# Optimization experiments

Measured on AMD Instinct MI355X. Metric: run time of the kernel, lower is better.

Reference implementation:

```python
import jax, jax.numpy as jnp
import numpy as np

N = 100000   # nodes in batched graph
E = 1600000  # edges (before self-loops)
D = 128      # in_dim == hidden_dim == num_outputs
G = 64       # graphs in the batch


def setup_inputs() -> dict:
    key = jax.random.key(0)
    ks = jax.random.split(key, 8)
    s = 1.0 / np.sqrt(D)
    x = jax.random.normal(ks[0], (N, D), jnp.float32)
    src = jax.random.randint(ks[1], (E,), 0, N, dtype=jnp.int64)
    dst = jax.random.randint(ks[2], (E,), 0, N, dtype=jnp.int64)
    graph_ids = jnp.sort(jax.random.randint(ks[3], (N,), 0, G, dtype=jnp.int64))
    W0 = jax.random.normal(ks[4], (D, D), jnp.float32) * s
    W1 = jax.random.normal(ks[5], (D, D), jnp.float32) * s
    W2 = jax.random.normal(ks[6], (D, D), jnp.float32) * s
    b0 = jnp.zeros((D,), jnp.float32)
    b1 = jnp.zeros((D,), jnp.float32)
    b2 = jnp.zeros((D,), jnp.float32)
    return {"x": x, "W0": W0, "b0": b0, "W1": W1, "b1": b1,
            "W2": W2, "b2": b2, "src": src, "dst": dst, "graph_ids": graph_ids}


def reference(x, W0, b0, W1, b1, W2, b2, src, dst, graph_ids):
    n = x.shape[0]
    loops = jnp.arange(n, dtype=src.dtype)
    src_f = jnp.concatenate([src, loops])  # add self-loops once (dgl.add_self_loop)
    dst_f = jnp.concatenate([dst, loops])
    ones_e = jnp.ones(src_f.shape, x.dtype)
    deg_out = jax.ops.segment_sum(ones_e, src_f, num_segments=n)  # >=1 (self-loop)
    deg_in = jax.ops.segment_sum(ones_e, dst_f, num_segments=n)
    cs = jax.lax.rsqrt(deg_out)[:, None]  # source norm (GraphConv norm='both')
    cd = jax.lax.rsqrt(deg_in)[:, None]   # destination norm

    def gcn_layer(h, W, b):
        m = (h * cs)[src_f]                                   # [E+N, D] gather
        agg = jax.ops.segment_sum(m, dst_f, num_segments=n)   # scatter-add SpMM
        return jax.nn.relu((agg * cd) @ W + b)                # F.relu(conv(g, h))

    h = gcn_layer(x, W0, b0)
    h = gcn_layer(h, W1, b1)
    h = gcn_layer(h, W2, b2)

    # dgl.mean_nodes: per-graph mean over nodes
    sums = jax.ops.segment_sum(h, graph_ids, num_segments=G)
    cnt = jax.ops.segment_sum(jnp.ones((n, 1), h.dtype), graph_ids, num_segments=G)
    return sums / jnp.maximum(cnt, 1.0)  # [G, D] logits
```

## Files before the change

### kernel.cpp

```cpp
#include <hip/hip_runtime.h>
#include <stdint.h>

#define D 128
#define CAP 64
#define HB 128
#define CH 25000

typedef __attribute__((ext_vector_type(8))) short bf16x8;
typedef __attribute__((ext_vector_type(4))) float f32x4;

__device__ inline unsigned short f2bf(float x) {
  union { float f; uint32_t u; } v; v.f = x;
  uint32_t u = v.u;
  u += 0x7fffu + ((u >> 16) & 1u);
  return (unsigned short)(u >> 16);
}
__device__ inline float bflo(uint32_t u) {
  union { uint32_t u; float f; } v; v.u = u << 16; return v.f;
}
__device__ inline float bfhi(uint32_t u) {
  union { uint32_t u; float f; } v; v.u = u & 0xffff0000u; return v.f;
}
__device__ inline uint32_t packbf(float lo, float hi) {
  return (uint32_t)f2bf(lo) | ((uint32_t)f2bf(hi) << 16);
}

__global__ __launch_bounds__(256) void hist_kernel(
    const int* __restrict__ src, const int* __restrict__ dst,
    unsigned int* __restrict__ parts_s, unsigned int* __restrict__ parts_d,
    int E, int N,
    const float* __restrict__ W0, const float* __restrict__ W1,
    const float* __restrict__ W2, unsigned short* __restrict__ Wt,
    int* __restrict__ cnt, int G, float* __restrict__ outz, int out_total) {
  __shared__ unsigned int lbs[CH / 8];
  __shared__ unsigned int lbd[CH / 8];
  int b = blockIdx.x & (HB - 1);
  int lo = (blockIdx.x >> 7) * CH;
  for (int i = threadIdx.x; i < CH / 8; i += 256) { lbs[i] = 0; lbd[i] = 0; }
  __syncthreads();
  int per = (E + HB - 1) / HB;
  int e0 = b * per;
  int e1 = min(e0 + per, E);
  for (int e = e0 + threadIdx.x; e < e1; e += 256) {
    int rs = src[e] - lo;
    if ((unsigned)rs < CH) atomicAdd(&lbs[rs >> 3], 1u << ((rs & 7) * 4));
    int rd = dst[e] - lo;
    if ((unsigned)rd < CH) atomicAdd(&lbd[rd >> 3], 1u << ((rd & 7) * 4));
  }
  __syncthreads();
  int nu = (N + 7) / 8;
  int base = lo >> 3;
  int cu = min(CH / 8, nu - base);
  unsigned int* ps = parts_s + (size_t)b * nu + base;
  unsigned int* pd = parts_d + (size_t)b * nu + base;
  for (int i = threadIdx.x; i < cu; i += 256) { ps[i] = lbs[i]; pd[i] = lbd[i]; }

  int gs = gridDim.x * 256;
  for (int i = blockIdx.x * 256 + threadIdx.x; i < 3 * 16384; i += gs) {
    int l = i >> 14, r = i & 16383;
    int n = r >> 7, k = r & 127;
    const float* W = (l == 0) ? W0 : (l == 1) ? W1 : W2;
    Wt[i] = f2bf(W[k * 128 + n]);
  }
  for (int i = blockIdx.x * 256 + threadIdx.x; i < G; i += gs) cnt[i] = 0;
  for (int i = blockIdx.x * 256 + threadIdx.x; i < out_total; i += gs) outz[i] = 0.f;
}

__global__ __launch_bounds__(256) void scan_norm_kernel(
    const unsigned char* __restrict__ parts_s,
    const unsigned char* __restrict__ parts_d,
    unsigned char* __restrict__ offs_d,
    int* __restrict__ degd,
    float* __restrict__ cs, float* __restrict__ cd,
    const int* __restrict__ gid, int* __restrict__ cnt,
    int N, int G) {
  __shared__ int lcnt[256];
  for (int i = threadIdx.x; i < G; i += 256) lcnt[i] = 0;
  __syncthreads();

  int t = blockIdx.x * blockDim.x + threadIdx.x;
  int i0 = t * 2;
  if (i0 < N) {
    int nb = N / 2;
    int ds0 = 0, ds1 = 0, dd0 = 0, dd1 = 0;
    for (int b = 0; b < HB; b++) {
      unsigned char sv = parts_s[(size_t)b * nb + t];
      ds0 += sv & 15; ds1 += sv >> 4;
      unsigned char dv = parts_d[(size_t)b * nb + t];
      offs_d[(size_t)b * N + i0]     = (unsigned char)min(dd0, 255);
      offs_d[(size_t)b * N + i0 + 1] = (unsigned char)min(dd1, 255);
      dd0 += dv & 15; dd1 += dv >> 4;
    }
    degd[i0] = dd0;     degd[i0 + 1] = dd1;
    cs[i0] = rsqrtf((float)ds0 + 1.0f);
    cs[i0 + 1] = rsqrtf((float)ds1 + 1.0f);
    cd[i0] = rsqrtf((float)dd0 + 1.0f);
    cd[i0 + 1] = rsqrtf((float)dd1 + 1.0f);
    atomicAdd(&lcnt[gid[i0]], 1);
    if (i0 + 1 < N) atomicAdd(&lcnt[gid[i0 + 1]], 1);
  }
  __syncthreads();
  for (int i = threadIdx.x; i < G; i += 256) {
    int c = lcnt[i];
    if (c) atomicAdd(&cnt[i], c);
  }
}

__global__ __launch_bounds__(256) void fill_kernel(
    const int* __restrict__ src, const int* __restrict__ dst,
    const unsigned char* __restrict__ offs_d, int* __restrict__ col, int E, int N,
    const float* __restrict__ x, const float* __restrict__ cs,
    uint32_t* __restrict__ xs) {
  __shared__ unsigned int lcur[CH / 8];
  int b = blockIdx.x & (HB - 1);
  int lo = (blockIdx.x >> 7) * CH;
  for (int i = threadIdx.x; i < CH / 8; i += 256) lcur[i] = 0;
  __syncthreads();
  int per = (E + HB - 1) / HB;
  int e0 = b * per;
  int e1 = min(e0 + per, E);
  const unsigned char* offb = offs_d + (size_t)b * N;
  for (int e = e0 + threadIdx.x; e < e1; e += 256) {
    int d = dst[e];
    int rd = d - lo;
    if ((unsigned)rd < CH) {
      unsigned old = atomicAdd(&lcur[rd >> 3], 1u << ((rd & 7) * 4));
      int local = (old >> ((rd & 7) * 4)) & 0xF;
      int pos = (int)offb[d] + local;
      if (pos < CAP) col[(size_t)d * CAP + pos] = src[e];
    }
  }
  int total2 = N * 64;
  int gs = gridDim.x * 256;
  for (int i = blockIdx.x * 256 + threadIdx.x; i < total2; i += gs) {
    float2 v = ((const float2*)x)[i];
    float c = cs[i >> 6];
    xs[i] = packbf(v.x * c, v.y * c);
  }
}

__global__ __launch_bounds__(512) void fused_layer_kernel(
    const uint32_t* __restrict__ hin, const unsigned short* __restrict__ Wt,
    const float* __restrict__ bias, const float* __restrict__ cd,
    const float* __restrict__ rowscale, const int* __restrict__ degd,
    const int* __restrict__ col, unsigned short* __restrict__ hout, int N) {
  __shared__ __align__(16) uint32_t At[16 * 68];

  int wv = threadIdx.x >> 6;
  int lane = threadIdx.x & 63;
  int m = lane & 15;
  int quad = lane >> 4;

  bf16x8 bfr[4];
#pragma unroll
  for (int c = 0; c < 4; c++)
    bfr[c] = *(const bf16x8*)(Wt + (size_t)(16 * wv + m) * 128 + c * 32 + quad * 8);

#pragma unroll
  for (int j = 0; j < 2; j++) {
    int w = __builtin_amdgcn_readfirstlane(blockIdx.x * 16 + wv * 2 + j);
    float accx = 0.f, accy = 0.f;
    if (w < N) {
      int n = min(degd[w], CAP);
      const int* cw = col + (size_t)w * CAP;
      const uint32_t* hl = hin + lane;
      uint32_t selfv = hl[(size_t)w * 64];
      accx = bflo(selfv); accy = bfhi(selfv);
      int i = 0;
      for (; i + 7 < n; i += 8) {
        int s0 = cw[i],     s1 = cw[i + 1], s2 = cw[i + 2], s3 = cw[i + 3];
        int s4 = cw[i + 4], s5 = cw[i + 5], s6 = cw[i + 6], s7 = cw[i + 7];
        uint32_t v0 = hl[(size_t)s0 * 64];
        uint32_t v1 = hl[(size_t)s1 * 64];
        uint32_t v2 = hl[(size_t)s2 * 64];
        uint32_t v3 = hl[(size_t)s3 * 64];
        uint32_t v4 = hl[(size_t)s4 * 64];
        uint32_t v5 = hl[(size_t)s5 * 64];
        uint32_t v6 = hl[(size_t)s6 * 64];
        uint32_t v7 = hl[(size_t)s7 * 64];
        accx += bflo(v0); accy += bfhi(v0);
        accx += bflo(v1); accy += bfhi(v1);
        accx += bflo(v2); accy += bfhi(v2);
        accx += bflo(v3); accy += bfhi(v3);
        accx += bflo(v4); accy += bfhi(v4);
        accx += bflo(v5); accy += bfhi(v5);
        accx += bflo(v6); accy += bfhi(v6);
        accx += bflo(v7); accy += bfhi(v7);
      }
      for (; i + 3 < n; i += 4) {
        int s0 = cw[i], s1 = cw[i + 1], s2 = cw[i + 2], s3 = cw[i + 3];
        uint32_t v0 = hl[(size_t)s0 * 64];
        uint32_t v1 = hl[(size_t)s1 * 64];
        uint32_t v2 = hl[(size_t)s2 * 64];
        uint32_t v3 = hl[(size_t)s3 * 64];
        accx += bflo(v0); accy += bfhi(v0);
        accx += bflo(v1); accy += bfhi(v1);
        accx += bflo(v2); accy += bfhi(v2);
        accx += bflo(v3); accy += bfhi(v3);
      }
      for (; i < n; i++) {
        uint32_t v = hl[(size_t)cw[i] * 64];
        accx += bflo(v); accy += bfhi(v);
      }
      float cdv = cd[w];
      accx *= cdv; accy *= cdv;
    }
    At[(wv * 2 + j) * 68 + lane] = packbf(accx, accy);
  }
  __syncthreads();

  const unsigned short* arow = (const unsigned short*)At + m * 136;
  f32x4 acc = f32x4{0.f, 0.f, 0.f, 0.f};
#pragma unroll
  for (int c = 0; c < 4; c++) {
    bf16x8 a = *(const bf16x8*)(arow + c * 32 + quad * 8);
    acc = __builtin_amdgcn_mfma_f32_16x16x32_bf16(a, bfr[c], acc, 0, 0, 0);
  }
  int colb = 16 * wv + m;
  float bv = bias[colb];
#pragma unroll
  for (int i = 0; i < 4; i++) {
    int r = blockIdx.x * 16 + quad * 4 + i;
    if (r < N) {
      float v = acc[i] + bv;
      v = v > 0.f ? v : 0.f;
      if (rowscale) v *= rowscale[r];
      hout[(size_t)r * D + colb] = f2bf(v);
    }
  }
}

__global__ void pool_kernel(const unsigned short* __restrict__ h, const int* __restrict__ gid,
                            float* __restrict__ outsum, const int* __restrict__ cnt, int N) {
  int v0 = blockIdx.x * 64;
  if (v0 >= N) return;
  int d = threadIdx.x;
  int vend = min(v0 + 64, N);
  int cur = gid[v0];
  float acc = 0.f;
  for (int v = v0; v < vend; v++) {
    int g = gid[v];
    if (g != cur) {
      float inv = 1.0f / fmaxf((float)cnt[cur], 1.0f);
      atomicAdd(&outsum[cur * D + d], acc * inv);
      acc = 0.f; cur = g;
    }
    unsigned short hv = __builtin_nontemporal_load(&h[(size_t)v * D + d]);
    union { uint32_t u; float f; } cv; cv.u = (uint32_t)hv << 16;
    acc += cv.f;
  }
  float inv = 1.0f / fmaxf((float)cnt[cur], 1.0f);
  atomicAdd(&outsum[cur * D + d], acc * inv);
}

extern "C" void kernel_launch(void* const* d_in, const int* in_sizes, int n_in,
                              void* d_out, int out_size, void* d_ws, size_t ws_size,
                              hipStream_t stream) {
  const float* x  = (const float*)d_in[0];
  const float* W0 = (const float*)d_in[1];
  const float* b0 = (const float*)d_in[2];
  const float* W1 = (const float*)d_in[3];
  const float* b1 = (const float*)d_in[4];
  const float* W2 = (const float*)d_in[5];
  const float* b2 = (const float*)d_in[6];
  const int* src  = (const int*)d_in[7];
  const int* dst  = (const int*)d_in[8];
  const int* gid  = (const int*)d_in[9];

  const int N = in_sizes[0] / D;
  const int E = in_sizes[7];
  const int G = out_size / D;
  const int nu = (N + 7) / 8;

  uint32_t* hsA = (uint32_t*)d_ws;
  uint32_t* hsB = hsA + (size_t)N * 64;
  int* col      = (int*)(hsB + (size_t)N * 64);
  int* degd     = col + (size_t)N * CAP;
  float* csb    = (float*)(degd + N);
  float* cdb    = csb + N;
  int* cnt      = (int*)(cdb + N);
  unsigned short* Wt = (unsigned short*)(cnt + G);
  unsigned int* parts_s = (unsigned int*)(Wt + 3 * 16384);
  unsigned int* parts_d = parts_s + (size_t)HB * nu;
  unsigned char* offs_d = (unsigned char*)(parts_d + (size_t)HB * nu);

  const int nch = (N + CH - 1) / CH;
  hist_kernel<<<HB * nch, 256, 0, stream>>>(src, dst, parts_s, parts_d, E, N,
                                            W0, W1, W2, Wt, cnt, G,
                                            (float*)d_out, out_size);
  scan_norm_kernel<<<(N / 2 + 255) / 256, 256, 0, stream>>>(
      (const unsigned char*)parts_s, (const unsigned char*)parts_d, offs_d,
      degd, csb, cdb, gid, cnt, N, G);
  fill_kernel<<<HB * nch, 256, 0, stream>>>(src, dst, offs_d, col, E, N, x, csb, hsA);

  const int ltiles = (N + 15) / 16;

  fused_layer_kernel<<<ltiles, 512, 0, stream>>>(hsA, Wt, b0, cdb, csb, degd, col,
                                                 (unsigned short*)hsB, N);
  fused_layer_kernel<<<ltiles, 512, 0, stream>>>(hsB, Wt + 16384, b1, cdb, csb, degd, col,
                                                 (unsigned short*)hsA, N);
  fused_layer_kernel<<<ltiles, 512, 0, stream>>>(hsA, Wt + 2 * 16384, b2, cdb, nullptr, degd, col,
                                                 (unsigned short*)hsB, N);

  pool_kernel<<<(N + 63) / 64, 128, 0, stream>>>((const unsigned short*)hsB, gid,
                                                 (float*)d_out, cnt, N);
}
```

Measured before the change: 454.1 us.

## Build adjacency with global atomics and broadcast neighbor indices via readlane

Replaces the three-kernel shared-memory histogram, scan and fill pipeline with a single kernel that uses global atomics to count degrees and place source indices into the capped per-destination column lists, plus a fused normalisation, x-scaling and weight-transpose kernel. The layer kernel now loads each node's 64 neighbor indices once per wave and broadcasts them with readlane, interleaving two destination rows to overlap their gathers, and it uses nontemporal stores for outputs. This removes kernel launches and the partition scratch traffic, at the cost of heavy global atomic contention and a nondeterministic neighbor order.

```diff
diff --git a/kernel.cpp b/kernel.cpp
--- a/kernel.cpp
+++ b/kernel.cpp
@@ -3,8 +3,6 @@
 
 #define D 128
 #define CAP 64
-#define HB 128
-#define CH 25000
 
 typedef __attribute__((ext_vector_type(8))) short bf16x8;
 typedef __attribute__((ext_vector_type(4))) float f32x4;
@@ -25,121 +23,71 @@
   return (uint32_t)f2bf(lo) | ((uint32_t)f2bf(hi) << 16);
 }
 
-__global__ __launch_bounds__(256) void hist_kernel(
+__global__ __launch_bounds__(256) void build_kernel(
     const int* __restrict__ src, const int* __restrict__ dst,
-    unsigned int* __restrict__ parts_s, unsigned int* __restrict__ parts_d,
-    int E, int N,
+    int* __restrict__ degs, int* __restrict__ degd, int* __restrict__ col, int E) {
+  int t = blockIdx.x * 256 + threadIdx.x;
+  int gs = gridDim.x * 256;
+  int half = E >> 1;
+  for (int i = t; i < half; i += gs) {
+    int2 s2 = ((const int2*)src)[i];
+    int2 d2 = ((const int2*)dst)[i];
+    atomicAdd(&degs[s2.x], 1);
+    atomicAdd(&degs[s2.y], 1);
+    int p0 = atomicAdd(&degd[d2.x], 1);
+    if (p0 < CAP) col[(size_t)d2.x * CAP + p0] = s2.x;
+    int p1 = atomicAdd(&degd[d2.y], 1);
+    if (p1 < CAP) col[(size_t)d2.y * CAP + p1] = s2.y;
+  }
+  if (t == 0 && (E & 1)) {
+    int e = E - 1;
+    int s = src[e], d = dst[e];
+    atomicAdd(&degs[s], 1);
+    int p = atomicAdd(&degd[d], 1);
+    if (p < CAP) col[(size_t)d * CAP + p] = s;
+  }
+}
+
+__global__ __launch_bounds__(256) void norm_x_kernel(
+    const float* __restrict__ x, const int* __restrict__ degs,
+    const int* __restrict__ degd, float* __restrict__ cs, float* __restrict__ cd,
+    uint2* __restrict__ xs4, const int* __restrict__ gid, int* __restrict__ cnt,
+    int N, int G,
     const float* __restrict__ W0, const float* __restrict__ W1,
-    const float* __restrict__ W2, unsigned short* __restrict__ Wt,
-    int* __restrict__ cnt, int G, float* __restrict__ outz, int out_total) {
-  __shared__ unsigned int lbs[CH / 8];
-  __shared__ unsigned int lbd[CH / 8];
-  int b = blockIdx.x & (HB - 1);
-  int lo = (blockIdx.x >> 7) * CH;
-  for (int i = threadIdx.x; i < CH / 8; i += 256) { lbs[i] = 0; lbd[i] = 0; }
+    const float* __restrict__ W2, unsigned short* __restrict__ Wt) {
+  __shared__ int lcnt[256];
+  int t = blockIdx.x * 256 + threadIdx.x;
+  int gs = gridDim.x * 256;
+  for (int i = threadIdx.x; i < G; i += 256) lcnt[i] = 0;
   __syncthreads();
-  int per = (E + HB - 1) / HB;
-  int e0 = b * per;
-  int e1 = min(e0 + per, E);
-  for (int e = e0 + threadIdx.x; e < e1; e += 256) {
-    int rs = src[e] - lo;
-    if ((unsigned)rs < CH) atomicAdd(&lbs[rs >> 3], 1u << ((rs & 7) * 4));
-    int rd = dst[e] - lo;
-    if ((unsigned)rd < CH) atomicAdd(&lbd[rd >> 3], 1u << ((rd & 7) * 4));
+  for (int i = t; i < N; i += gs) {
+    cs[i] = rsqrtf((float)degs[i] + 1.0f);
+    cd[i] = rsqrtf((float)degd[i] + 1.0f);
+    atomicAdd(&lcnt[gid[i]], 1);
   }
   __syncthreads();
-  int nu = (N + 7) / 8;
-  int base = lo >> 3;
-  int cu = min(CH / 8, nu - base);
-  unsigned int* ps = parts_s + (size_t)b * nu + base;
-  unsigned int* pd = parts_d + (size_t)b * nu + base;
-  for (int i = threadIdx.x; i < cu; i += 256) { ps[i] = lbs[i]; pd[i] = lbd[i]; }
-
-  int gs = gridDim.x * 256;
-  for (int i = blockIdx.x * 256 + threadIdx.x; i < 3 * 16384; i += gs) {
+  for (int i = threadIdx.x; i < G; i += 256) {
+    int c = lcnt[i];
+    if (c) atomicAdd(&cnt[i], c);
+  }
+  int tot = N * 32;
+  for (int i = t; i < tot; i += gs) {
+    float4 v = ((const float4*)x)[i];
+    float c = rsqrtf((float)degs[i >> 5] + 1.0f);
+    uint2 o;
+    o.x = packbf(v.x * c, v.y * c);
+    o.y = packbf(v.z * c, v.w * c);
+    xs4[i] = o;
+  }
+  for (int i = t; i < 3 * 16384; i += gs) {
     int l = i >> 14, r = i & 16383;
     int n = r >> 7, k = r & 127;
     const float* W = (l == 0) ? W0 : (l == 1) ? W1 : W2;
     Wt[i] = f2bf(W[k * 128 + n]);
   }
-  for (int i = blockIdx.x * 256 + threadIdx.x; i < G; i += gs) cnt[i] = 0;
-  for (int i = blockIdx.x * 256 + threadIdx.x; i < out_total; i += gs) outz[i] = 0.f;
-}
-
-__global__ __launch_bounds__(256) void scan_norm_kernel(
-    const unsigned char* __restrict__ parts_s,
-    const unsigned char* __restrict__ parts_d,
-    unsigned char* __restrict__ offs_d,
-    int* __restrict__ degd,
-    float* __restrict__ cs, float* __restrict__ cd,
-    const int* __restrict__ gid, int* __restrict__ cnt,
-    int N, int G) {
-  __shared__ int lcnt[256];
-  for (int i = threadIdx.x; i < G; i += 256) lcnt[i] = 0;
-  __syncthreads();
-
-  int t = blockIdx.x * blockDim.x + threadIdx.x;
-  int i0 = t * 2;
-  if (i0 < N) {
-    int nb = N / 2;
-    int ds0 = 0, ds1 = 0, dd0 = 0, dd1 = 0;
-    for (int b = 0; b < HB; b++) {
-      unsigned char sv = parts_s[(size_t)b * nb + t];
-      ds0 += sv & 15; ds1 += sv >> 4;
-      unsigned char dv = parts_d[(size_t)b * nb + t];
-      offs_d[(size_t)b * N + i0]     = (unsigned char)min(dd0, 255);
-      offs_d[(size_t)b * N + i0 + 1] = (unsigned char)min(dd1, 255);
-      dd0 += dv & 15; dd1 += dv >> 4;
-    }
-    degd[i0] = dd0;     degd[i0 + 1] = dd1;
-    cs[i0] = rsqrtf((float)ds0 + 1.0f);
-    cs[i0 + 1] = rsqrtf((float)ds1 + 1.0f);
-    cd[i0] = rsqrtf((float)dd0 + 1.0f);
-    cd[i0 + 1] = rsqrtf((float)dd1 + 1.0f);
-    atomicAdd(&lcnt[gid[i0]], 1);
-    if (i0 + 1 < N) atomicAdd(&lcnt[gid[i0 + 1]], 1);
-  }
-  __syncthreads();
-  for (int i = threadIdx.x; i < G; i += 256) {
-    int c = lcnt[i];
-    if (c) atomicAdd(&cnt[i], c);
-  }
-}
-
-__global__ __launch_bounds__(256) void fill_kernel(
-    const int* __restrict__ src, const int* __restrict__ dst,
-    const unsigned char* __restrict__ offs_d, int* __restrict__ col, int E, int N,
-    const float* __restrict__ x, const float* __restrict__ cs,
-    uint32_t* __restrict__ xs) {
-  __shared__ unsigned int lcur[CH / 8];
-  int b = blockIdx.x & (HB - 1);
-  int lo = (blockIdx.x >> 7) * CH;
-  for (int i = threadIdx.x; i < CH / 8; i += 256) lcur[i] = 0;
-  __syncthreads();
-  int per = (E + HB - 1) / HB;
-  int e0 = b * per;
-  int e1 = min(e0 + per, E);
-  const unsigned char* offb = offs_d + (size_t)b * N;
-  for (int e = e0 + threadIdx.x; e < e1; e += 256) {
-    int d = dst[e];
-    int rd = d - lo;
-    if ((unsigned)rd < CH) {
-      unsigned old = atomicAdd(&lcur[rd >> 3], 1u << ((rd & 7) * 4));
-      int local = (old >> ((rd & 7) * 4)) & 0xF;
-      int pos = (int)offb[d] + local;
-      if (pos < CAP) col[(size_t)d * CAP + pos] = src[e];
-    }
-  }
-  int total2 = N * 64;
-  int gs = gridDim.x * 256;
-  for (int i = blockIdx.x * 256 + threadIdx.x; i < total2; i += gs) {
-    float2 v = ((const float2*)x)[i];
-    float c = cs[i >> 6];
-    xs[i] = packbf(v.x * c, v.y * c);
-  }
-}
-
-__global__ __launch_bounds__(512) void fused_layer_kernel(
+}
+
+__global__ __launch_bounds__(512, 8) void fused_layer_kernel(
     const uint32_t* __restrict__ hin, const unsigned short* __restrict__ Wt,
     const float* __restrict__ bias, const float* __restrict__ cd,
     const float* __restrict__ rowscale, const int* __restrict__ degd,
@@ -156,57 +104,94 @@
   for (int c = 0; c < 4; c++)
     bfr[c] = *(const bf16x8*)(Wt + (size_t)(16 * wv + m) * 128 + c * 32 + quad * 8);
 
-#pragma unroll
-  for (int j = 0; j < 2; j++) {
-    int w = __builtin_amdgcn_readfirstlane(blockIdx.x * 16 + wv * 2 + j);
-    float accx = 0.f, accy = 0.f;
-    if (w < N) {
-      int n = min(degd[w], CAP);
-      const int* cw = col + (size_t)w * CAP;
-      const uint32_t* hl = hin + lane;
-      uint32_t selfv = hl[(size_t)w * 64];
-      accx = bflo(selfv); accy = bfhi(selfv);
-      int i = 0;
-      for (; i + 7 < n; i += 8) {
-        int s0 = cw[i],     s1 = cw[i + 1], s2 = cw[i + 2], s3 = cw[i + 3];
-        int s4 = cw[i + 4], s5 = cw[i + 5], s6 = cw[i + 6], s7 = cw[i + 7];
-        uint32_t v0 = hl[(size_t)s0 * 64];
-        uint32_t v1 = hl[(size_t)s1 * 64];
-        uint32_t v2 = hl[(size_t)s2 * 64];
-        uint32_t v3 = hl[(size_t)s3 * 64];
-        uint32_t v4 = hl[(size_t)s4 * 64];
-        uint32_t v5 = hl[(size_t)s5 * 64];
-        uint32_t v6 = hl[(size_t)s6 * 64];
-        uint32_t v7 = hl[(size_t)s7 * 64];
-        accx += bflo(v0); accy += bfhi(v0);
-        accx += bflo(v1); accy += bfhi(v1);
-        accx += bflo(v2); accy += bfhi(v2);
-        accx += bflo(v3); accy += bfhi(v3);
-        accx += bflo(v4); accy += bfhi(v4);
-        accx += bflo(v5); accy += bfhi(v5);
-        accx += bflo(v6); accy += bfhi(v6);
-        accx += bflo(v7); accy += bfhi(v7);
-      }
-      for (; i + 3 < n; i += 4) {
-        int s0 = cw[i], s1 = cw[i + 1], s2 = cw[i + 2], s3 = cw[i + 3];
-        uint32_t v0 = hl[(size_t)s0 * 64];
-        uint32_t v1 = hl[(size_t)s1 * 64];
-        uint32_t v2 = hl[(size_t)s2 * 64];
-        uint32_t v3 = hl[(size_t)s3 * 64];
-        accx += bflo(v0); accy += bfhi(v0);
-        accx += bflo(v1); accy += bfhi(v1);
-        accx += bflo(v2); accy += bfhi(v2);
-        accx += bflo(v3); accy += bfhi(v3);
-      }
-      for (; i < n; i++) {
-        uint32_t v = hl[(size_t)cw[i] * 64];
-        accx += bflo(v); accy += bfhi(v);
-      }
-      float cdv = cd[w];
-      accx *= cdv; accy *= cdv;
-    }
-    At[(wv * 2 + j) * 68 + lane] = packbf(accx, accy);
-  }
+  int w0 = blockIdx.x * 16 + wv * 2;
+  int w1 = w0 + 1;
+  float ax0 = 0.f, ay0 = 0.f, ax1 = 0.f, ay1 = 0.f;
+  int n0 = 0, n1 = 0;
+  int idx0 = 0, idx1 = 0;
+  if (w0 < N) {
+    n0 = min(degd[w0], CAP);
+    idx0 = __builtin_nontemporal_load(&col[(size_t)w0 * CAP + lane]);
+    uint32_t sv = hin[(size_t)w0 * 64 + lane];
+    ax0 = bflo(sv); ay0 = bfhi(sv);
+  }
+  if (w1 < N) {
+    n1 = min(degd[w1], CAP);
+    idx1 = __builtin_nontemporal_load(&col[(size_t)w1 * CAP + lane]);
+    uint32_t sv = hin[(size_t)w1 * 64 + lane];
+    ax1 = bflo(sv); ay1 = bfhi(sv);
+  }
+  const uint32_t* hl = hin + lane;
+  int i0 = 0, i1 = 0;
+  while (i0 + 8 <= n0 && i1 + 8 <= n1) {
+    uint32_t v0[8], v1[8];
+#pragma unroll
+    for (int k = 0; k < 8; k++) {
+      int s = __builtin_amdgcn_readlane(idx0, i0 + k);
+      v0[k] = hl[(size_t)s * 64];
+    }
+#pragma unroll
+    for (int k = 0; k < 8; k++) {
+      int s = __builtin_amdgcn_readlane(idx1, i1 + k);
+      v1[k] = hl[(size_t)s * 64];
+    }
+#pragma unroll
+    for (int k = 0; k < 8; k++) { ax0 += bflo(v0[k]); ay0 += bfhi(v0[k]); }
+#pragma unroll
+    for (int k = 0; k < 8; k++) { ax1 += bflo(v1[k]); ay1 += bfhi(v1[k]); }
+    i0 += 8; i1 += 8;
+  }
+  while (i0 + 8 <= n0) {
+    uint32_t v[8];
+#pragma unroll
+    for (int k = 0; k < 8; k++) {
+      int s = __builtin_amdgcn_readlane(idx0, i0 + k);
+      v[k] = hl[(size_t)s * 64];
+    }
+#pragma unroll
+    for (int k = 0; k < 8; k++) { ax0 += bflo(v[k]); ay0 += bfhi(v[k]); }
+    i0 += 8;
+  }
+  if (i0 < n0) {
+    uint32_t v[8];
+#pragma unroll
+    for (int k = 0; k < 8; k++) {
+      if (i0 + k < n0) {
+        int s = __builtin_amdgcn_readlane(idx0, i0 + k);
+        v[k] = hl[(size_t)s * 64];
+      } else v[k] = 0;
+    }
+#pragma unroll
+    for (int k = 0; k < 8; k++) { ax0 += bflo(v[k]); ay0 += bfhi(v[k]); }
+  }
+  while (i1 + 8 <= n1) {
+    uint32_t v[8];
+#pragma unroll
+    for (int k = 0; k < 8; k++) {
+      int s = __builtin_amdgcn_readlane(idx1, i1 + k);
+      v[k] = hl[(size_t)s * 64];
+    }
+#pragma unroll
+    for (int k = 0; k < 8; k++) { ax1 += bflo(v[k]); ay1 += bfhi(v[k]); }
+    i1 += 8;
+  }
+  if (i1 < n1) {
+    uint32_t v[8];
+#pragma unroll
+    for (int k = 0; k < 8; k++) {
+      if (i1 + k < n1) {
+        int s = __builtin_amdgcn_readlane(idx1, i1 + k);
+        v[k] = hl[(size_t)s * 64];
+      } else v[k] = 0;
+    }
+#pragma unroll
+    for (int k = 0; k < 8; k++) { ax1 += bflo(v[k]); ay1 += bfhi(v[k]); }
+  }
+
+  if (w0 < N) { float c = cd[w0]; ax0 *= c; ay0 *= c; }
+  if (w1 < N) { float c = cd[w1]; ax1 *= c; ay1 *= c; }
+  At[(wv * 2 + 0) * 68 + lane] = packbf(ax0, ay0);
+  At[(wv * 2 + 1) * 68 + lane] = packbf(ax1, ay1);
   __syncthreads();
 
   const unsigned short* arow = (const unsigned short*)At + m * 136;
@@ -225,7 +210,7 @@
       float v = acc[i] + bv;
       v = v > 0.f ? v : 0.f;
       if (rowscale) v *= rowscale[r];
-      hout[(size_t)r * D + colb] = f2bf(v);
+      __builtin_nontemporal_store(f2bf(v), &hout[(size_t)r * D + colb]);
     }
   }
 }
@@ -270,28 +255,25 @@
   const int N = in_sizes[0] / D;
   const int E = in_sizes[7];
   const int G = out_size / D;
-  const int nu = (N + 7) / 8;
 
   uint32_t* hsA = (uint32_t*)d_ws;
   uint32_t* hsB = hsA + (size_t)N * 64;
   int* col      = (int*)(hsB + (size_t)N * 64);
-  int* degd     = col + (size_t)N * CAP;
-  float* csb    = (float*)(degd + N);
+  int* degs     = col + (size_t)N * CAP;
+  int* degd     = degs + N;
+  int* cnt      = degd + N;
+  float* csb    = (float*)(cnt + G);
   float* cdb    = csb + N;
-  int* cnt      = (int*)(cdb + N);
-  unsigned short* Wt = (unsigned short*)(cnt + G);
-  unsigned int* parts_s = (unsigned int*)(Wt + 3 * 16384);
-  unsigned int* parts_d = parts_s + (size_t)HB * nu;
-  unsigned char* offs_d = (unsigned char*)(parts_d + (size_t)HB * nu);
-
-  const int nch = (N + CH - 1) / CH;
-  hist_kernel<<<HB * nch, 256, 0, stream>>>(src, dst, parts_s, parts_d, E, N,
-                                            W0, W1, W2, Wt, cnt, G,
-                                            (float*)d_out, out_size);
-  scan_norm_kernel<<<(N / 2 + 255) / 256, 256, 0, stream>>>(
-      (const unsigned char*)parts_s, (const unsigned char*)parts_d, offs_d,
-      degd, csb, cdb, gid, cnt, N, G);
-  fill_kernel<<<HB * nch, 256, 0, stream>>>(src, dst, offs_d, col, E, N, x, csb, hsA);
+  unsigned short* Wt = (unsigned short*)(cdb + N);
+
+  hipMemsetAsync(degs, 0, (size_t)(2 * N + G) * sizeof(int), stream);
+  hipMemsetAsync(d_out, 0, (size_t)out_size * sizeof(float), stream);
+
+  int bgrid = min((E / 2 + 255) / 256, 4096);
+  if (bgrid < 1) bgrid = 1;
+  build_kernel<<<bgrid, 256, 0, stream>>>(src, dst, degs, degd, col, E);
+  norm_x_kernel<<<2048, 256, 0, stream>>>(x, degs, degd, csb, cdb, (uint2*)hsA,
+                                          gid, cnt, N, G, W0, W1, W2, Wt);
 
   const int ltiles = (N + 15) / 16;
 
```

Measured after the change: 597.4 us. 1.32x slower.
